# Kernel optimization log

Hardware: AMD Instinct MI355X
Metric: run time of the kernel (lower is better)

Reference implementation:

```python
import jax, jax.numpy as jnp
import numpy as np
from jax import lax

T, B, IN, H0, H1 = 512, 1024, 32, 128, 64


def _lstm_cell(x, h, c, Wih, Whh, bih, bhh):
    # PyTorch LSTMCell: gates ordered i, f, g, o
    gates = x @ Wih.T + bih + h @ Whh.T + bhh  # [B, 4H]
    i, f, g, o = jnp.split(gates, 4, axis=-1)
    i = jax.nn.sigmoid(i)
    f = jax.nn.sigmoid(f)
    g = jnp.tanh(g)
    o = jax.nn.sigmoid(o)
    c2 = f * c + i * g
    h2 = o * jnp.tanh(c2)
    return h2, c2


def setup_inputs() -> dict:
    key = jax.random.key(0)
    ks = jax.random.split(key, 12)

    def u(k, shape, fan_in):
        bound = 1.0 / np.sqrt(fan_in)
        return jax.random.uniform(k, shape, jnp.float32, -bound, bound)

    inp = {
        "x": jax.random.normal(ks[0], (T, B, IN), jnp.float32),
        "h0": jnp.zeros((B, H0), jnp.float32),
        "c0": jnp.zeros((B, H0), jnp.float32),
        "h1": jnp.zeros((B, H1), jnp.float32),
        "c1": jnp.zeros((B, H1), jnp.float32),
        # layer 0 LSTMCell (input 32 -> hidden 128)
        "W_ih0": u(ks[1], (4 * H0, IN), H0),
        "W_hh0": u(ks[2], (4 * H0, H0), H0),
        "b_ih0": u(ks[3], (4 * H0,), H0),
        "b_hh0": u(ks[4], (4 * H0,), H0),
        # layer 0 shortcut Linear (32 -> 128)
        "Ws0": u(ks[5], (H0, IN), IN),
        "bs0": u(ks[6], (H0,), IN),
        # layer 1 LSTMCell (input 128 -> hidden 64)
        "W_ih1": u(ks[7], (4 * H1, H0), H1),
        "W_hh1": u(ks[8], (4 * H1, H1), H1),
        "b_ih1": u(ks[9], (4 * H1,), H1),
        "b_hh1": u(ks[10], (4 * H1,), H1),
        # layer 1 shortcut Linear (128 -> 64)
        "Ws1": u(ks[11], (H1, H0), H0),
        "bs1": jnp.zeros((H1,), jnp.float32),
    }
    return inp


def reference(x, h0, c0, h1, c1,
              W_ih0, W_hh0, b_ih0, b_hh0, Ws0, bs0,
              W_ih1, W_hh1, b_ih1, b_hh1, Ws1, bs1):
    def step(carry, xt):
        h0, c0, h1, c1 = carry
        # layer 0: hx[0] aliases out, so in-place residual add lands in the
        # carried state (post-residual, PRE-clip); clipped value feeds layer 1.
        out0, c0 = _lstm_cell(xt, h0, c0, W_ih0, W_hh0, b_ih0, b_hh0)
        h0 = out0 + xt @ Ws0.T + bs0
        inp1 = jnp.clip(h0, -10, 10)
        # layer 1
        out1, c1 = _lstm_cell(inp1, h1, c1, W_ih1, W_hh1, b_ih1, b_hh1)
        h1 = out1 + inp1 @ Ws1.T + bs1
        y = jnp.clip(h1, -10, 10)
        return (h0, c0, h1, c1), y

    (h0, c0, h1, c1), ys = lax.scan(step, (h0, c0, h1, c1), x)
    return ys, h0, c0, h1, c1
```

## Files before the change

### kernel.cpp

```cpp
#include <hip/hip_runtime.h>
#include <cstdint>
#include <cstddef>

namespace {

constexpr int TS  = 512;
constexpr int BB  = 1024;
constexpr int IND = 32;
constexpr int H0D = 128;
constexpr int H1D = 64;
constexpr int RPW = 4;
constexpr int S0  = 132;
constexpr int S1  = 68;

typedef float f32x4 __attribute__((ext_vector_type(4)));
typedef __bf16 bf16x8 __attribute__((ext_vector_type(8)));

__device__ __forceinline__ float rcpf(float x) {
    float r; asm("v_rcp_f32 %0, %1" : "=v"(r) : "v"(x)); return r;
}
__device__ __forceinline__ float sigm(float z) { return rcpf(1.0f + __expf(-z)); }
__device__ __forceinline__ float tanh_f(float z) {
    return fmaf(-2.0f, rcpf(__expf(2.0f * z) + 1.0f), 1.0f);
}
__device__ __forceinline__ bf16x8 cvt8(f32x4 a, f32x4 b) {
    bf16x8 r;
    r[0] = (__bf16)a[0]; r[1] = (__bf16)a[1]; r[2] = (__bf16)a[2]; r[3] = (__bf16)a[3];
    r[4] = (__bf16)b[0]; r[5] = (__bf16)b[1]; r[6] = (__bf16)b[2]; r[7] = (__bf16)b[3];
    return r;
}
__device__ __forceinline__ bf16x8 ld8(const float* p) {
    f32x4 a = *(const f32x4*)p;
    f32x4 b = *(const f32x4*)(p + 4);
    return cvt8(a, b);
}
__device__ __forceinline__ f32x4 mfma16(bf16x8 a, bf16x8 b, f32x4 c) {
    return __builtin_amdgcn_mfma_f32_16x16x32_bf16(a, b, c, 0, 0, 0);
}

__global__ __launch_bounds__(512, 2) void resid_lstm(
    const float* __restrict__ x,
    const float* __restrict__ h0i, const float* __restrict__ c0i,
    const float* __restrict__ h1i, const float* __restrict__ c1i,
    const float* __restrict__ Wih0, const float* __restrict__ Whh0,
    const float* __restrict__ bih0, const float* __restrict__ bhh0,
    const float* __restrict__ Ws0,  const float* __restrict__ bs0v,
    const float* __restrict__ Wih1, const float* __restrict__ Whh1,
    const float* __restrict__ bih1, const float* __restrict__ bhh1,
    const float* __restrict__ Ws1,  const float* __restrict__ bs1v,
    float* __restrict__ out)
{
    const int tid  = threadIdx.x;
    const int lane = tid & 63;
    const int w    = tid >> 6;
    const int fr   = lane & 15;
    const int fk   = lane >> 4;
    const int row0 = blockIdx.x * RPW;
    const bool prod = (w < 4);

    __shared__ __align__(16) float h0f[2][RPW][S0];
    __shared__ __align__(16) float i1f[2][RPW][S0];
    __shared__ __align__(16) float h1q[2][RPW][S1];

    for (int i = tid; i < 2 * RPW * S0; i += 512) {
        (&h0f[0][0][0])[i] = 0.f;
        (&i1f[0][0][0])[i] = 0.f;
    }
    for (int i = tid; i < 2 * RPW * S1; i += 512)
        (&h1q[0][0][0])[i] = 0.f;
    __syncthreads();

    bf16x8 WF[42];
    float BZ[10];
    float CS[2];
    CS[0] = 0.f; CS[1] = 0.f;

    if (prod) {
        #pragma unroll
        for (int sl = 0; sl < 2; ++sl) {
            const int u = (w + 4*sl)*16 + fr;
            #pragma unroll
            for (int g = 0; g < 4; ++g) {
                const int r0 = g*H0D + u;
                WF[sl*21 + g*5] = ld8(Wih0 + r0*IND + fk*8);
                #pragma unroll
                for (int ks = 0; ks < 4; ++ks)
                    WF[sl*21 + g*5 + 1 + ks] = ld8(Whh0 + r0*H0D + ks*32 + fk*8);
                BZ[sl*5 + g] = bih0[r0] + bhh0[r0];
            }
            WF[sl*21 + 20] = ld8(Ws0 + u*IND + fk*8);
            BZ[sl*5 + 4] = bs0v[u];
            CS[sl] = c0i[(size_t)(row0 + fk)*H0D + u];
        }
    } else {
        const int u1 = (w - 4)*16 + fr;
        #pragma unroll
        for (int g = 0; g < 4; ++g) {
            const int r1 = g*H1D + u1;
            #pragma unroll
            for (int ks = 0; ks < 4; ++ks)
                WF[g*6 + ks] = ld8(Wih1 + r1*H0D + ks*32 + fk*8);
            #pragma unroll
            for (int k2 = 0; k2 < 2; ++k2)
                WF[g*6 + 4 + k2] = ld8(Whh1 + r1*H1D + k2*32 + fk*8);
            BZ[g] = bih1[r1] + bhh1[r1];
        }
        #pragma unroll
        for (int ks = 0; ks < 4; ++ks)
            WF[24 + ks] = ld8(Ws1 + u1*H0D + ks*32 + fk*8);
        BZ[4] = bs1v[u1];
        CS[0] = c1i[(size_t)(row0 + fk)*H1D + u1];
    }

    {
        const int u = tid & 127, b2 = tid >> 7;
        h0f[0][b2][u] = h0i[(size_t)(row0 + b2)*H0D + u];
    }
    if (tid < RPW * H1D) {
        const int u = tid & 63, b2 = tid >> 6;
        h1q[0][b2][u] = h1i[(size_t)(row0 + b2)*H1D + u];
    }

    const int arow = fr >> 2;

    const float* xbase = x + ((size_t)row0 + arow)*IND + fk*8;
    f32x4 xa = {0,0,0,0}, xb = {0,0,0,0};
    if (prod) { xa = *(const f32x4*)xbase; xb = *(const f32x4*)(xbase + 4); }

    __syncthreads();

    const size_t H0O = (size_t)TS*BB*H1D;
    const size_t C0O = H0O + (size_t)BB*H0D;
    const size_t H1O = C0O + (size_t)BB*H0D;
    const size_t C1O = H1O + (size_t)BB*H1D;

    #pragma unroll 1
    for (int t = 0; t < TS; ++t) {
        const int rp = t & 1;
        if (prod) {
            bf16x8 xf = cvt8(xa, xb);
            {
                const int tn = (t + 1 < TS) ? (t + 1) : t;
                const float* xp = xbase + (size_t)tn * (BB*IND);
                xa = *(const f32x4*)xp; xb = *(const f32x4*)(xp + 4);
            }
            bf16x8 hf[4];
            #pragma unroll
            for (int ks = 0; ks < 4; ++ks)
                hf[ks] = ld8(&h0f[rp][arow][ks*32 + fk*8]);

            #pragma unroll
            for (int sl = 0; sl < 2; ++sl) {
                const int u = (w + 4*sl)*16 + fr;
                f32x4 ag[5];
                #pragma unroll
                for (int g = 0; g < 4; ++g) {
                    const float b = BZ[sl*5 + g];
                    f32x4 a = {b, b, b, b};
                    a = mfma16(xf, WF[sl*21 + g*5], a);
                    #pragma unroll
                    for (int ks = 0; ks < 4; ++ks)
                        a = mfma16(hf[ks], WF[sl*21 + g*5 + 1 + ks], a);
                    ag[g] = a;
                }
                {
                    const float b = BZ[sl*5 + 4];
                    f32x4 a = {b, b, b, b};
                    ag[4] = mfma16(xf, WF[sl*21 + 20], a);
                }
                const float i_ = sigm(ag[0][0]);
                const float f_ = sigm(ag[1][0]);
                const float g_ = tanh_f(ag[2][0]);
                const float o_ = sigm(ag[3][0]);
                const float c  = fmaf(f_, CS[sl], i_ * g_);
                CS[sl] = c;
                const float hn = fmaf(o_, tanh_f(c), ag[4][0]);
                const float iv = fminf(fmaxf(hn, -10.f), 10.f);
                h0f[rp ^ 1][fk][u] = hn;
                i1f[rp ^ 1][fk][u] = iv;
                if (t == TS - 1) {
                    out[H0O + (size_t)(row0 + fk)*H0D + u] = hn;
                    out[C0O + (size_t)(row0 + fk)*H0D + u] = c;
                }
            }
        }
        __syncthreads();

        if (!prod) {
            bf16x8 pf[4], hq[2];
            #pragma unroll
            for (int ks = 0; ks < 4; ++ks)
                pf[ks] = ld8(&i1f[rp ^ 1][arow][ks*32 + fk*8]);
            #pragma unroll
            for (int k2 = 0; k2 < 2; ++k2)
                hq[k2] = ld8(&h1q[rp][arow][k2*32 + fk*8]);

            const int u1 = (w - 4)*16 + fr;
            f32x4 a1[5];
            #pragma unroll
            for (int g = 0; g < 4; ++g) {
                const float b = BZ[g];
                f32x4 a = {b, b, b, b};
                #pragma unroll
                for (int ks = 0; ks < 4; ++ks)
                    a = mfma16(pf[ks], WF[g*6 + ks], a);
                #pragma unroll
                for (int k2 = 0; k2 < 2; ++k2)
                    a = mfma16(hq[k2], WF[g*6 + 4 + k2], a);
                a1[g] = a;
            }
            {
                const float b = BZ[4];
                f32x4 a = {b, b, b, b};
                #pragma unroll
                for (int ks = 0; ks < 4; ++ks)
                    a = mfma16(pf[ks], WF[24 + ks], a);
                a1[4] = a;
            }
            const float i_ = sigm(a1[0][0]);
            const float f_ = sigm(a1[1][0]);
            const float g_ = tanh_f(a1[2][0]);
            const float o_ = sigm(a1[3][0]);
            const float c  = fmaf(f_, CS[0], i_ * g_);
            CS[0] = c;
            const float hn = fmaf(o_, tanh_f(c), a1[4][0]);
            const float yv = fminf(fmaxf(hn, -10.f), 10.f);
            out[((size_t)t*BB + row0 + fk)*H1D + u1] = yv;
            h1q[rp ^ 1][fk][u1] = hn;
            if (t == TS - 1) {
                out[H1O + (size_t)(row0 + fk)*H1D + u1] = hn;
                out[C1O + (size_t)(row0 + fk)*H1D + u1] = c;
            }
        }
    }
}

}

extern "C" void kernel_launch(void* const* d_in, const int* in_sizes, int n_in,
                              void* d_out, int out_size, void* d_ws, size_t ws_size,
                              hipStream_t stream) {
    (void)in_sizes; (void)n_in; (void)d_ws; (void)ws_size; (void)out_size;
    const float* x    = (const float*)d_in[0];
    const float* h0i  = (const float*)d_in[1];
    const float* c0i  = (const float*)d_in[2];
    const float* h1i  = (const float*)d_in[3];
    const float* c1i  = (const float*)d_in[4];
    const float* Wih0 = (const float*)d_in[5];
    const float* Whh0 = (const float*)d_in[6];
    const float* bih0 = (const float*)d_in[7];
    const float* bhh0 = (const float*)d_in[8];
    const float* Ws0  = (const float*)d_in[9];
    const float* bs0  = (const float*)d_in[10];
    const float* Wih1 = (const float*)d_in[11];
    const float* Whh1 = (const float*)d_in[12];
    const float* bih1 = (const float*)d_in[13];
    const float* bhh1 = (const float*)d_in[14];
    const float* Ws1  = (const float*)d_in[15];
    const float* bs1  = (const float*)d_in[16];

    resid_lstm<<<dim3(BB / RPW), dim3(512), 0, stream>>>(
        x, h0i, c0i, h1i, c1i,
        Wih0, Whh0, bih0, bhh0, Ws0, bs0,
        Wih1, Whh1, bih1, bhh1, Ws1, bs1,
        (float*)d_out);
}
```

Before: 602.0 us.

## Split layer-0 hidden units across eight waves instead of four per block

Raises the block size from 512 to 768 threads so layer 0 uses eight producer waves, each owning one 16-unit slice instead of two. This halves the per-wave MFMA chain and weight registers on the layer-0 critical path (WF shrinks from 42 to 28 entries). The launch bound becomes (768, 3) to keep per-wave register pressure bounded. The cost is more waves per block and barrier participants, which may reduce blocks resident per CU.

```diff
diff --git a/kernel.cpp b/kernel.cpp
--- a/kernel.cpp
+++ b/kernel.cpp
@@ -12,6 +12,7 @@
 constexpr int RPW = 4;
 constexpr int S0  = 132;
 constexpr int S1  = 68;
+constexpr int NT  = 768;
 
 typedef float f32x4 __attribute__((ext_vector_type(4)));
 typedef __bf16 bf16x8 __attribute__((ext_vector_type(8)));
@@ -38,7 +39,7 @@
     return __builtin_amdgcn_mfma_f32_16x16x32_bf16(a, b, c, 0, 0, 0);
 }
 
-__global__ __launch_bounds__(512, 2) void resid_lstm(
+__global__ __launch_bounds__(NT, 3) void resid_lstm(
     const float* __restrict__ x,
     const float* __restrict__ h0i, const float* __restrict__ c0i,
     const float* __restrict__ h1i, const float* __restrict__ c1i,
@@ -56,44 +57,40 @@
     const int fr   = lane & 15;
     const int fk   = lane >> 4;
     const int row0 = blockIdx.x * RPW;
-    const bool prod = (w < 4);
+    const bool prod = (w < 8);
 
     __shared__ __align__(16) float h0f[2][RPW][S0];
     __shared__ __align__(16) float i1f[2][RPW][S0];
     __shared__ __align__(16) float h1q[2][RPW][S1];
 
-    for (int i = tid; i < 2 * RPW * S0; i += 512) {
+    for (int i = tid; i < 2 * RPW * S0; i += NT) {
         (&h0f[0][0][0])[i] = 0.f;
         (&i1f[0][0][0])[i] = 0.f;
     }
-    for (int i = tid; i < 2 * RPW * S1; i += 512)
+    for (int i = tid; i < 2 * RPW * S1; i += NT)
         (&h1q[0][0][0])[i] = 0.f;
     __syncthreads();
 
-    bf16x8 WF[42];
-    float BZ[10];
-    float CS[2];
-    CS[0] = 0.f; CS[1] = 0.f;
+    bf16x8 WF[28];
+    float BZ[5];
+    float CS = 0.f;
 
     if (prod) {
+        const int u = w*16 + fr;
         #pragma unroll
-        for (int sl = 0; sl < 2; ++sl) {
-            const int u = (w + 4*sl)*16 + fr;
-            #pragma unroll
-            for (int g = 0; g < 4; ++g) {
-                const int r0 = g*H0D + u;
-                WF[sl*21 + g*5] = ld8(Wih0 + r0*IND + fk*8);
-                #pragma unroll
-                for (int ks = 0; ks < 4; ++ks)
-                    WF[sl*21 + g*5 + 1 + ks] = ld8(Whh0 + r0*H0D + ks*32 + fk*8);
-                BZ[sl*5 + g] = bih0[r0] + bhh0[r0];
-            }
-            WF[sl*21 + 20] = ld8(Ws0 + u*IND + fk*8);
-            BZ[sl*5 + 4] = bs0v[u];
-            CS[sl] = c0i[(size_t)(row0 + fk)*H0D + u];
-        }
+        for (int g = 0; g < 4; ++g) {
+            const int r0 = g*H0D + u;
+            WF[g*5] = ld8(Wih0 + r0*IND + fk*8);
+            #pragma unroll
+            for (int ks = 0; ks < 4; ++ks)
+                WF[g*5 + 1 + ks] = ld8(Whh0 + r0*H0D + ks*32 + fk*8);
+            BZ[g] = bih0[r0] + bhh0[r0];
+        }
+        WF[20] = ld8(Ws0 + u*IND + fk*8);
+        BZ[4] = bs0v[u];
+        CS = c0i[(size_t)(row0 + fk)*H0D + u];
     } else {
-        const int u1 = (w - 4)*16 + fr;
+        const int u1 = (w - 8)*16 + fr;
         #pragma unroll
         for (int g = 0; g < 4; ++g) {
             const int r1 = g*H1D + u1;
@@ -109,10 +106,10 @@
         for (int ks = 0; ks < 4; ++ks)
             WF[24 + ks] = ld8(Ws1 + u1*H0D + ks*32 + fk*8);
         BZ[4] = bs1v[u1];
-        CS[0] = c1i[(size_t)(row0 + fk)*H1D + u1];
-    }
-
-    {
+        CS = c1i[(size_t)(row0 + fk)*H1D + u1];
+    }
+
+    if (tid < RPW * H0D) {
         const int u = tid & 127, b2 = tid >> 7;
         h0f[0][b2][u] = h0i[(size_t)(row0 + b2)*H0D + u];
     }
@@ -149,39 +146,36 @@
             for (int ks = 0; ks < 4; ++ks)
                 hf[ks] = ld8(&h0f[rp][arow][ks*32 + fk*8]);
 
-            #pragma unroll
-            for (int sl = 0; sl < 2; ++sl) {
-                const int u = (w + 4*sl)*16 + fr;
-                f32x4 ag[5];
-                #pragma unroll
-                for (int g = 0; g < 4; ++g) {
-                    const float b = BZ[sl*5 + g];
-                    f32x4 a = {b, b, b, b};
-                    a = mfma16(xf, WF[sl*21 + g*5], a);
-                    #pragma unroll
-                    for (int ks = 0; ks < 4; ++ks)
-                        a = mfma16(hf[ks], WF[sl*21 + g*5 + 1 + ks], a);
-                    ag[g] = a;
-                }
-                {
-                    const float b = BZ[sl*5 + 4];
-                    f32x4 a = {b, b, b, b};
-                    ag[4] = mfma16(xf, WF[sl*21 + 20], a);
-                }
-                const float i_ = sigm(ag[0][0]);
-                const float f_ = sigm(ag[1][0]);
-                const float g_ = tanh_f(ag[2][0]);
-                const float o_ = sigm(ag[3][0]);
-                const float c  = fmaf(f_, CS[sl], i_ * g_);
-                CS[sl] = c;
-                const float hn = fmaf(o_, tanh_f(c), ag[4][0]);
-                const float iv = fminf(fmaxf(hn, -10.f), 10.f);
-                h0f[rp ^ 1][fk][u] = hn;
-                i1f[rp ^ 1][fk][u] = iv;
-                if (t == TS - 1) {
-                    out[H0O + (size_t)(row0 + fk)*H0D + u] = hn;
-                    out[C0O + (size_t)(row0 + fk)*H0D + u] = c;
-                }
+            const int u = w*16 + fr;
+            f32x4 ag[5];
+            #pragma unroll
+            for (int g = 0; g < 4; ++g) {
+                const float b = BZ[g];
+                f32x4 a = {b, b, b, b};
+                a = mfma16(xf, WF[g*5], a);
+                #pragma unroll
+                for (int ks = 0; ks < 4; ++ks)
+                    a = mfma16(hf[ks], WF[g*5 + 1 + ks], a);
+                ag[g] = a;
+            }
+            {
+                const float b = BZ[4];
+                f32x4 a = {b, b, b, b};
+                ag[4] = mfma16(xf, WF[20], a);
+            }
+            const float i_ = sigm(ag[0][0]);
+            const float f_ = sigm(ag[1][0]);
+            const float g_ = tanh_f(ag[2][0]);
+            const float o_ = sigm(ag[3][0]);
+            const float c  = fmaf(f_, CS, i_ * g_);
+            CS = c;
+            const float hn = fmaf(o_, tanh_f(c), ag[4][0]);
+            const float iv = fminf(fmaxf(hn, -10.f), 10.f);
+            h0f[rp ^ 1][fk][u] = hn;
+            i1f[rp ^ 1][fk][u] = iv;
+            if (t == TS - 1) {
+                out[H0O + (size_t)(row0 + fk)*H0D + u] = hn;
+                out[C0O + (size_t)(row0 + fk)*H0D + u] = c;
             }
         }
         __syncthreads();
@@ -195,7 +189,7 @@
             for (int k2 = 0; k2 < 2; ++k2)
                 hq[k2] = ld8(&h1q[rp][arow][k2*32 + fk*8]);
 
-            const int u1 = (w - 4)*16 + fr;
+            const int u1 = (w - 8)*16 + fr;
             f32x4 a1[5];
             #pragma unroll
             for (int g = 0; g < 4; ++g) {
@@ -221,8 +215,8 @@
             const float f_ = sigm(a1[1][0]);
             const float g_ = tanh_f(a1[2][0]);
             const float o_ = sigm(a1[3][0]);
-            const float c  = fmaf(f_, CS[0], i_ * g_);
-            CS[0] = c;
+            const float c  = fmaf(f_, CS, i_ * g_);
+            CS = c;
             const float hn = fmaf(o_, tanh_f(c), a1[4][0]);
             const float yv = fminf(fmaxf(hn, -10.f), 10.f);
             out[((size_t)t*BB + row0 + fk)*H1D + u1] = yv;
@@ -259,7 +253,7 @@
     const float* Ws1  = (const float*)d_in[15];
     const float* bs1  = (const float*)d_in[16];
 
-    resid_lstm<<<dim3(BB / RPW), dim3(512), 0, stream>>>(
+    resid_lstm<<<dim3(BB / RPW), dim3(NT), 0, stream>>>(
         x, h0i, c0i, h1i, c1i,
         Wih0, Whh0, bih0, bhh0, Ws0, bs0,
         Wih1, Whh1, bih1, bhh1, Ws1, bs1,
```

Measured after the change: 782.7 us. +30.0%, slower.
